# Performance work log

Measured on AMD Instinct MI355X. Metric: run time of the kernel, lower is better.

Reference implementation:

```python
import jax, jax.numpy as jnp
import numpy as np

NUM_EXPERTS = 16
TOP_K = 2


def _swiglu(x, w13, w2):
    # x: [t, d]; w13: [2I, d] (gate and up fused); w2: [d, I]
    h = x @ w13.T                      # [t, 2I]
    gate, up = jnp.split(h, 2, axis=-1)
    return (jax.nn.silu(gate) * up) @ w2.T  # [t, d]


def setup_inputs() -> dict:
    key = jax.random.key(0)
    ks = jax.random.split(key, 6)
    T, D, I, E, SI = 4096, 1024, 512, NUM_EXPERTS, 2048
    return {
        "hidden_states": jax.random.normal(ks[0], (T, D), jnp.float32),
        "router_logits": jax.random.normal(ks[1], (T, E), jnp.float32),
        "w13": jax.random.normal(ks[2], (E, 2 * I, D), jnp.float32) * (1.0 / np.sqrt(D)),
        "w2": jax.random.normal(ks[3], (E, D, I), jnp.float32) * (1.0 / np.sqrt(I)),
        "w13_shared": jax.random.normal(ks[4], (2 * SI, D), jnp.float32) * (1.0 / np.sqrt(D)),
        "w2_shared": jax.random.normal(ks[5], (D, SI), jnp.float32) * (1.0 / np.sqrt(SI)),
    }


def reference(hidden_states, router_logits, w13, w2, w13_shared, w2_shared):
    # Shared expert path (overlapped with routed dispatch in the original).
    shared_out = _swiglu(hidden_states, w13_shared, w2_shared)  # [T, d]

    # Routing: softmax -> top-k -> renormalize (vLLM FusedMoE w/ renormalize=True).
    probs = jax.nn.softmax(router_logits, axis=-1)              # [T, E]
    topk_w, topk_idx = jax.lax.top_k(probs, TOP_K)              # [T, k]
    topk_w = topk_w / jnp.sum(topk_w, axis=-1, keepdims=True)

    # Dense combine-weight matrix [T, E]: zero where expert not selected.
    T = hidden_states.shape[0]
    combine = jnp.zeros((T, NUM_EXPERTS), hidden_states.dtype)
    combine = combine.at[jnp.arange(T)[:, None], topk_idx].add(topk_w)

    # Grouped expert compute: scan over experts (fixed structural set),
    # accumulating the combine-weighted SwiGLU output. Memory-friendly: no
    # [E, T, 2I] intermediate is materialized.
    def body(acc, ew):
        w13_e, w2_e, c_e = ew                     # [2I,d], [d,I], [T]
        y = _swiglu(hidden_states, w13_e, w2_e)   # [T, d]
        return acc + c_e[:, None] * y, None

    fused_out, _ = jax.lax.scan(body, jnp.zeros_like(hidden_states),
                                (w13, w2, combine.T))
    return shared_out, fused_out
```

## Files before the change

### kernel.cpp

```cpp
#include <hip/hip_runtime.h>


#define T_TOK 4096
#define NEXP  16

typedef __attribute__((ext_vector_type(8))) short   short8;
typedef __attribute__((ext_vector_type(4))) float   floatx4;

typedef __attribute__((address_space(1))) void as1_void;
typedef __attribute__((address_space(3))) void as3_void;

__device__ __forceinline__ float bf2f(ushort u) {
    union { unsigned int i; float f; } v; v.i = ((unsigned int)u) << 16; return v.f;
}
__device__ __forceinline__ ushort f2bf(float f) {
    unsigned int u = __builtin_bit_cast(unsigned int, f);
    unsigned int r = 0x7FFFu + ((u >> 16) & 1u);
    return (ushort)((u + r) >> 16);
}

__device__ __forceinline__ float load_elem(const void* p, long i, int bf) {
    return bf ? bf2f(((const ushort*)p)[i]) : ((const float*)p)[i];
}

__device__ __forceinline__ void top2(const void* logits, int t, int bf,
                                     int& b0, int& b1, float& w0, float& w1) {
    float l[16];
#pragma unroll
    for (int j = 0; j < 16; ++j) l[j] = load_elem(logits, t * 16 + j, bf);
    b0 = 0; float v0 = l[0];
#pragma unroll
    for (int j = 1; j < 16; ++j) { if (l[j] > v0) { v0 = l[j]; b0 = j; } }
    b1 = -1; float v1 = -3.4e38f;
#pragma unroll
    for (int j = 0; j < 16; ++j) {
        if (j == b0) continue;
        if (l[j] > v1) { v1 = l[j]; b1 = j; }
    }
    float d = __expf(v1 - v0);
    w0 = 1.0f / (1.0f + d);
    w1 = d / (1.0f + d);
}

__global__ __launch_bounds__(1024)
void setup_all(const void* __restrict__ in0, const void* __restrict__ in4,
               const void* __restrict__ logits,
               int* __restrict__ dflag, int* __restrict__ xsel,
               int* __restrict__ counts, int* __restrict__ offsets,
               int* __restrict__ pairinfo, float* __restrict__ pairw)
{
    __shared__ int   s_cnt[16], s_off[16], s_cur[16];
    __shared__ int   s_dcnt, s_dflag, s_xsel;
    __shared__ float s0s, s4s;
    const int tid = threadIdx.x;

    if (tid < 16) { s_cnt[tid] = 0; s_cur[tid] = 0; }
    if (tid == 0) { s_dcnt = 0; s0s = 0.f; s4s = 0.f; }
    __syncthreads();

    if (tid < 256) {
        const ushort* xu = (const ushort*)in0;
        int ok = 0;
        for (int i = tid; i < 512; i += 256) {
            int e = (xu[2 * i] >> 7) & 0xFF;
            ok += (e >= 90 && e <= 140) ? 1 : 0;
        }
        atomicAdd(&s_dcnt, ok);
    }
    __syncthreads();
    if (tid == 0) { s_dflag = (s_dcnt >= 384) ? 1 : 0; *dflag = s_dflag; }
    __syncthreads();
    const int bf = s_dflag;

    if (tid < 256) {
        float a0 = 0.f, a4 = 0.f;
        for (int i = tid; i < 4096; i += 256) {
            a0 += fabsf(load_elem(in0, (long)i * 997 + 13, bf));
            a4 += fabsf(load_elem(in4, (long)i * 997 + 13, bf));
        }
        atomicAdd(&s0s, a0);
        atomicAdd(&s4s, a4);
    }
    __syncthreads();
    if (tid == 0) { s_xsel = (s0s >= s4s) ? 0 : 1; *xsel = s_xsel; }

    int   b0[4], b1[4];
    float w0[4], w1[4];
#pragma unroll
    for (int it = 0; it < 4; ++it) {
        const int t = tid + it * 1024;
        top2(logits, t, bf, b0[it], b1[it], w0[it], w1[it]);
        atomicAdd(&s_cnt[b0[it]], 1);
        atomicAdd(&s_cnt[b1[it]], 1);
    }
    __syncthreads();

    if (tid == 0) {
        int acc = 0;
        for (int e = 0; e < NEXP; ++e) {
            s_off[e] = acc; offsets[e] = acc; counts[e] = s_cnt[e];
            acc += s_cnt[e];
        }
    }
    __syncthreads();

#pragma unroll
    for (int it = 0; it < 4; ++it) {
        const int t = tid + it * 1024;
        int p0 = s_off[b0[it]] + atomicAdd(&s_cur[b0[it]], 1);
        pairinfo[p0] = 2 * t;     pairw[p0] = w0[it];
        int p1 = s_off[b1[it]] + atomicAdd(&s_cur[b1[it]], 1);
        pairinfo[p1] = 2 * t + 1; pairw[p1] = w1[it];
    }
}

__global__ __launch_bounds__(256)
void conv_all(const void* __restrict__ in0, const void* __restrict__ in4,
              const void* __restrict__ w13, const void* __restrict__ w2,
              const void* __restrict__ w2s, ushort* __restrict__ dst,
              const int* __restrict__ dflag, const int* __restrict__ xsel)
{
    const int bf = *dflag, xs = *xsel;
    const long E0 = 524288;
    const long E1 = 1048576;
    const long E2 = 3145728;
    const long E3 = 4194304;
    const long E4 = 4456448;
    long i = (long)blockIdx.x * blockDim.x + threadIdx.x;
    const long stride = (long)gridDim.x * blockDim.x;
    for (; i < E4; i += stride) {
        const void* src; long j;
        if      (i < E0) { src = xs ? in4 : in0; j = i;      }
        else if (i < E1) { src = xs ? in0 : in4; j = i - E0; }
        else if (i < E2) { src = w13;            j = i - E1; }
        else if (i < E3) { src = w2;             j = i - E2; }
        else             { src = w2s;            j = i - E3; }
        uint4 v;
        if (bf) {
            v = ((const uint4*)src)[j];
        } else {
            float4 f0 = ((const float4*)src)[j * 2];
            float4 f1 = ((const float4*)src)[j * 2 + 1];
            v.x = (unsigned)f2bf(f0.x) | ((unsigned)f2bf(f0.y) << 16);
            v.y = (unsigned)f2bf(f0.z) | ((unsigned)f2bf(f0.w) << 16);
            v.z = (unsigned)f2bf(f1.x) | ((unsigned)f2bf(f1.y) << 16);
            v.w = (unsigned)f2bf(f1.z) | ((unsigned)f2bf(f1.w) << 16);
        }
        ((uint4*)dst)[i] = v;
    }
}

__global__ void to_bf16(const void* __restrict__ pA, const void* __restrict__ pB,
                        ushort* __restrict__ dst, long n8,
                        const int* __restrict__ dflag, const int* __restrict__ xsel)
{
    const void* src = (pB != nullptr && *xsel) ? pB : pA;
    const int bf = *dflag;
    long i = (long)blockIdx.x * blockDim.x + threadIdx.x;
    const long stride = (long)gridDim.x * blockDim.x;
    for (; i < n8; i += stride) {
        uint4 v;
        if (bf) {
            v = ((const uint4*)src)[i];
        } else {
            float4 f0 = ((const float4*)src)[i * 2];
            float4 f1 = ((const float4*)src)[i * 2 + 1];
            v.x = (unsigned)f2bf(f0.x) | ((unsigned)f2bf(f0.y) << 16);
            v.y = (unsigned)f2bf(f0.z) | ((unsigned)f2bf(f0.w) << 16);
            v.z = (unsigned)f2bf(f1.x) | ((unsigned)f2bf(f1.y) << 16);
            v.w = (unsigned)f2bf(f1.z) | ((unsigned)f2bf(f1.w) << 16);
        }
        ((uint4*)dst)[i] = v;
    }
}

__device__ __forceinline__ void gload16(const ushort* g, ushort* l) {
    __builtin_amdgcn_global_load_lds((as1_void*)g, (as3_void*)l, 16, 0, 0);
}

template <int SWIGLU, int GATHER, int ROUTED, int SCATTER, int NARROW = 0>
__device__ __forceinline__ void gemm_core(
    ushort* __restrict__ smem,
    const ushort* __restrict__ A, int lda,
    const ushort* __restrict__ B0, long upoff, long bbase, int ldb,
    void* __restrict__ C, int ldc, float* __restrict__ C2,
    int m0, int n0, int Mloc, int K, int pair_base,
    const int* __restrict__ pairinfo, const float* __restrict__ pairw)
{
    constexpr int BNRW = (SWIGLU || NARROW);
    constexpr int NBI = BNRW ? 2 : 4;
    constexpr int NFN = BNRW ? 2 : 4;

    ushort* As  = smem;
    ushort* Bs0 = smem + 128 * 64;
    ushort* Bs1 = SWIGLU ? (smem + 128 * 64 + 64 * 64) : nullptr;

    const int tid  = threadIdx.x;
    const int lane = tid & 63;
    const int wave = tid >> 6;
    const int srow = lane >> 3;
    const int scol = ((lane & 7) ^ srow) * 8;

    long aoff[4];
#pragma unroll
    for (int i = 0; i < 4; ++i) {
        int rl  = m0 + (wave * 4 + i) * 8 + srow;
        int rlc = rl < Mloc ? rl : Mloc - 1;
        long gr;
        if (GATHER)      gr = (long)(pairinfo[pair_base + rlc] >> 1);
        else if (ROUTED) gr = pair_base + rlc;
        else             gr = rlc;
        aoff[i] = gr * (long)lda + scol;
    }
    long boff[NBI];
#pragma unroll
    for (int i = 0; i < NBI; ++i) {
        int r = (wave * NBI + i) * 8 + srow;
        boff[i] = bbase + (long)(n0 + r) * ldb + scol;
    }

    const int wm   = (wave >> 1) * 64;
    const int wn   = (wave & 1) * (BNRW ? 32 : 64);
    const int r16  = lane & 15;
    const int quad = lane >> 4;
    const int rlow = r16 & 7;

    const floatx4 z4 = {0.f, 0.f, 0.f, 0.f};
    floatx4 accg[4][NFN], accu[4][NFN];
#pragma unroll
    for (int mi = 0; mi < 4; ++mi)
#pragma unroll
        for (int ni = 0; ni < NFN; ++ni) { accg[mi][ni] = z4; accu[mi][ni] = z4; }

    for (int k0 = 0; k0 < K; k0 += 64) {
#pragma unroll
        for (int i = 0; i < 4; ++i)
            gload16(A + aoff[i] + k0, &As[(wave * 4 + i) * 512]);
#pragma unroll
        for (int i = 0; i < NBI; ++i) {
            gload16(B0 + boff[i] + k0, &Bs0[(wave * NBI + i) * 512]);
            if constexpr (SWIGLU)
                gload16(B0 + boff[i] + upoff + k0, &Bs1[(wave * NBI + i) * 512]);
        }
        __syncthreads();
#pragma unroll
        for (int kc = 0; kc < 2; ++kc) {
            const int sw = ((kc * 4 + quad) ^ rlow) * 8;
            short8 af[4];
#pragma unroll
            for (int mi = 0; mi < 4; ++mi)
                af[mi] = *(const short8*)&As[(wm + mi * 16 + r16) * 64 + sw];
            short8 bfr[NFN], ufr[NFN];
#pragma unroll
            for (int ni = 0; ni < NFN; ++ni) {
                bfr[ni] = *(const short8*)&Bs0[(wn + ni * 16 + r16) * 64 + sw];
                if constexpr (SWIGLU)
                    ufr[ni] = *(const short8*)&Bs1[(wn + ni * 16 + r16) * 64 + sw];
            }
#pragma unroll
            for (int mi = 0; mi < 4; ++mi)
#pragma unroll
                for (int ni = 0; ni < NFN; ++ni) {
                    accg[mi][ni] = __builtin_amdgcn_mfma_f32_16x16x32_bf16(
                        af[mi], bfr[ni], accg[mi][ni], 0, 0, 0);
                    if constexpr (SWIGLU)
                        accu[mi][ni] = __builtin_amdgcn_mfma_f32_16x16x32_bf16(
                            af[mi], ufr[ni], accu[mi][ni], 0, 0, 0);
                }
        }
        __syncthreads();
    }

#pragma unroll
    for (int mi = 0; mi < 4; ++mi) {
#pragma unroll
        for (int r = 0; r < 4; ++r) {
            const int grow = m0 + wm + mi * 16 + quad * 4 + r;
            if (grow >= Mloc) continue;
            int info = 0; float w = 0.f;
            if constexpr (SCATTER) {
                const int p = pair_base + grow;
                info = pairinfo[p]; w = pairw[p];
            }
#pragma unroll
            for (int ni = 0; ni < NFN; ++ni) {
                const int col = n0 + wn + ni * 16 + r16;
                float val;
                if constexpr (SWIGLU) {
                    float g = accg[mi][ni][r];
                    float u = accu[mi][ni][r];
                    val = (g / (1.0f + __expf(-g))) * u;
                } else {
                    val = accg[mi][ni][r];
                }
                if constexpr (SCATTER) {
                    long idx = (long)(info >> 1) * 1024 + col;
                    float* dst = (info & 1) ? C2 : (float*)C;
                    dst[idx] = w * val;
                } else if constexpr (SWIGLU) {
                    long crow = ROUTED ? (long)(pair_base + grow) : (long)grow;
                    ((ushort*)C)[crow * ldc + col] = f2bf(val);
                } else {
                    ((float*)C)[(long)grow * ldc + col] = val;
                }
            }
        }
    }
}

template <int SWIGLU, int GATHER, int ROUTED, int SCATTER>
__global__ __launch_bounds__(256)
void gemm_fast(const ushort* __restrict__ A, int lda,
               const ushort* __restrict__ B0, long upoff, long strideB, int ldb,
               void* __restrict__ C, int ldc, float* __restrict__ C2,
               int M, int K,
               const int* __restrict__ counts, const int* __restrict__ offsets,
               const int* __restrict__ pairinfo, const float* __restrict__ pairw)
{
    __shared__ __align__(16) ushort smem[16384];
    const int e    = ROUTED ? (int)blockIdx.z : 0;
    const int Mloc = ROUTED ? counts[e] : M;
    const int m0   = blockIdx.y * 128;
    if (m0 >= Mloc) return;
    constexpr int BN = SWIGLU ? 64 : 128;
    const int n0  = blockIdx.x * BN;
    const int pb  = ROUTED ? offsets[e] : 0;
    const long bb = ROUTED ? (long)e * strideB : 0L;
    gemm_core<SWIGLU, GATHER, ROUTED, SCATTER>(
        smem, A, lda, B0, upoff, bb, ldb, C, ldc, C2,
        m0, n0, Mloc, K, pb, pairinfo, pairw);
}

__global__ __launch_bounds__(256)
void g1_fused(const ushort* __restrict__ hidb, const ushort* __restrict__ w13b,
              const ushort* __restrict__ w13sb,
              ushort* __restrict__ actR, ushort* __restrict__ actS,
              const int* __restrict__ counts, const int* __restrict__ offsets,
              const int* __restrict__ pairinfo)
{
    __shared__ __align__(16) ushort smem[16384];
    const int z  = blockIdx.z;
    const int m0 = blockIdx.y * 128;
    if (z < 4) {
        const int e    = z * 4 + ((int)blockIdx.x >> 3);
        const int Mloc = counts[e];
        if (m0 >= Mloc) return;
        const int n0 = ((int)blockIdx.x & 7) * 64;
        gemm_core<1, 1, 1, 0>(smem, hidb, 1024,
                              w13b, (long)512 * 1024, (long)e * 1024 * 1024, 1024,
                              actR, 512, nullptr,
                              m0, n0, Mloc, 1024, offsets[e], pairinfo, nullptr);
    } else {
        const int n0 = (int)blockIdx.x * 64;
        gemm_core<1, 0, 0, 0>(smem, hidb, 1024,
                              w13sb, (long)2048 * 1024, 0L, 1024,
                              actS, 2048, nullptr,
                              m0, n0, T_TOK, 1024, 0, nullptr, nullptr);
    }
}

template <int SPLIT>
__global__ __launch_bounds__(256)
void g2_fused(const ushort* __restrict__ actR, const ushort* __restrict__ actS,
              const ushort* __restrict__ w2b, const ushort* __restrict__ w2sb,
              float* __restrict__ outF, float* __restrict__ outT,
              float* __restrict__ outS, float* __restrict__ outP,
              const int* __restrict__ counts, const int* __restrict__ offsets,
              const int* __restrict__ pairinfo, const float* __restrict__ pairw)
{
    __shared__ __align__(16) ushort smem[16384];
    const int z  = blockIdx.z;
    const int m0 = blockIdx.y * 128;
    if (z < 4) {
        const int e    = z * 4 + ((int)blockIdx.x >> 3);
        const int Mloc = counts[e];
        if (m0 >= Mloc) return;
        const int n0 = ((int)blockIdx.x & 7) * 128;
        gemm_core<0, 0, 1, 1>(smem, actR, 512,
                              w2b, 0L, (long)e * 1024 * 512, 512,
                              outF, 1024, outT,
                              m0, n0, Mloc, 512, offsets[e], pairinfo, pairw);
    } else if constexpr (SPLIT) {
        const int zz = z - 4;
        if ((int)blockIdx.x >= 16) return;
        const int n0 = (int)blockIdx.x * 64;
        gemm_core<0, 0, 0, 0, 1>(smem, actS + zz * 1024, 2048,
                                 w2sb + zz * 1024, 0L, 0L, 2048,
                                 zz ? outP : outS, 1024, nullptr,
                                 m0, n0, T_TOK, 1024, 0, nullptr, nullptr);
    } else {
        if ((int)blockIdx.x >= 8) return;
        const int n0 = (int)blockIdx.x * 128;
        gemm_core<0, 0, 0, 0>(smem, actS, 2048,
                              w2sb, 0L, 0L, 2048,
                              outS, 1024, nullptr,
                              m0, n0, T_TOK, 2048, 0, nullptr, nullptr);
    }
}

__global__ void add_kernel(float* __restrict__ outF, const float* __restrict__ outT, int n4) {
    int i = blockIdx.x * blockDim.x + threadIdx.x;
    if (i >= n4) return;
    float4 a = *(const float4*)(outF + (long)i * 4);
    float4 b = *(const float4*)(outT + (long)i * 4);
    a.x += b.x; a.y += b.y; a.z += b.z; a.w += b.w;
    *(float4*)(outF + (long)i * 4) = a;
}

__global__ void add2_kernel(float* __restrict__ outF, const float* __restrict__ outT,
                            float* __restrict__ outS, const float* __restrict__ outP,
                            int n4) {
    int i = blockIdx.x * blockDim.x + threadIdx.x;
    if (i < n4) {
        float4 a = *(const float4*)(outF + (long)i * 4);
        float4 b = *(const float4*)(outT + (long)i * 4);
        a.x += b.x; a.y += b.y; a.z += b.z; a.w += b.w;
        *(float4*)(outF + (long)i * 4) = a;
    } else if (i < 2 * n4) {
        int j = i - n4;
        float4 a = *(const float4*)(outS + (long)j * 4);
        float4 b = *(const float4*)(outP + (long)j * 4);
        a.x += b.x; a.y += b.y; a.z += b.z; a.w += b.w;
        *(float4*)(outS + (long)j * 4) = a;
    }
}

__device__ __forceinline__ void stage8(const void* __restrict__ src, long eoff, int bf,
                                       ushort* __restrict__ dst) {
    if (bf) {
        *(uint4*)dst = *(const uint4*)((const ushort*)src + eoff);
    } else {
        const float* s = (const float*)src + eoff;
        float4 f0 = *(const float4*)s;
        float4 f1 = *(const float4*)(s + 4);
        uint4 v;
        v.x = (unsigned)f2bf(f0.x) | ((unsigned)f2bf(f0.y) << 16);
        v.y = (unsigned)f2bf(f0.z) | ((unsigned)f2bf(f0.w) << 16);
        v.z = (unsigned)f2bf(f1.x) | ((unsigned)f2bf(f1.y) << 16);
        v.w = (unsigned)f2bf(f1.z) | ((unsigned)f2bf(f1.w) << 16);
        *(uint4*)dst = v;
    }
}

template <int SWIGLU, int GATHER, int ROUTED, int SCATTER, int LOCAL,
          int A_DT, int B_DT, int C_F32>
__global__ __launch_bounds__(256)
void gemm_nt(const void* __restrict__ A, const void* __restrict__ Aalt, int lda,
             const void* __restrict__ B0, const void* __restrict__ B0alt,
             long upoff, long strideB,
             void* __restrict__ C, int ldc, void* __restrict__ C2,
             int M, int K, int row0,
             const int* __restrict__ dflag, const int* __restrict__ xsel,
             const int* __restrict__ counts, const int* __restrict__ offsets,
             const int* __restrict__ pairinfo, const float* __restrict__ pairw,
             int e_base, int m_base, int Mcap)
{
    const int dfl = (A_DT && B_DT) ? 1 : *dflag;
    const int abf = A_DT ? 1 : dfl;
    const int bbf = B_DT ? 1 : dfl;
    if (Aalt  && *xsel) A  = Aalt;
    if (B0alt && *xsel) B0 = B0alt;

    const int e = ROUTED ? (e_base + (int)blockIdx.z) : 0;
    int Mloc;
    if (ROUTED) {
        int avail = counts[e] - m_base;
        Mloc = avail < Mcap ? avail : Mcap;
    } else {
        Mloc = M;
    }
    const int m0 = blockIdx.y * 64;
    if (m0 >= Mloc) return;
    const int n0 = blockIdx.x * 64;
    const int pair_base = ROUTED ? (offsets[e] + m_base) : 0;
    const int abase     = ROUTED ? (LOCAL ? 0 : offsets[e]) : 0;
    const long bbase    = ROUTED ? (long)e * strideB : 0L;

    constexpr int LS = 72;
    __shared__ __align__(16) ushort As[64 * LS];
    __shared__ __align__(16) ushort Bs0[64 * LS];
    __shared__ __align__(16) ushort Bs1[SWIGLU ? 64 * LS : 8];

    const int tid = threadIdx.x;

    int  lofs[2];
    long aoff[2], boff[2];
#pragma unroll
    for (int i = 0; i < 2; ++i) {
        int idx = tid + i * 256;
        int row = idx >> 3;
        int col = (idx & 7) * 8;
        lofs[i] = row * LS + col;
        int rl  = m0 + row;
        int rlc = rl < Mloc ? rl : (Mloc - 1);
        long rA;
        if (GATHER)      rA = (long)(pairinfo[pair_base + rlc] >> 1);
        else if (ROUTED) rA = abase + rlc;
        else             rA = row0 + rl;
        aoff[i] = rA * (long)lda + col;
        boff[i] = bbase + (long)(n0 + row) * K + col;
    }

    const int lane = tid & 63;
    const int wave = tid >> 6;
    const int wm   = (wave >> 1) * 32;
    const int wn   = (wave & 1) * 32;
    const int r16  = lane & 15;
    const int quad = lane >> 4;

    floatx4 accg[2][2] = {{{0.f,0.f,0.f,0.f},{0.f,0.f,0.f,0.f}},{{0.f,0.f,0.f,0.f},{0.f,0.f,0.f,0.f}}};
    floatx4 accu[2][2] = {{{0.f,0.f,0.f,0.f},{0.f,0.f,0.f,0.f}},{{0.f,0.f,0.f,0.f},{0.f,0.f,0.f,0.f}}};

    for (int k0 = 0; k0 < K; k0 += 64) {
#pragma unroll
        for (int i = 0; i < 2; ++i) {
            stage8(A,  aoff[i] + k0, abf, &As[lofs[i]]);
            stage8(B0, boff[i] + k0, bbf, &Bs0[lofs[i]]);
            if (SWIGLU) stage8(B0, boff[i] + k0 + upoff, bbf, &Bs1[lofs[i]]);
        }
        __syncthreads();
#pragma unroll
        for (int kc = 0; kc < 2; ++kc) {
            const int kof = kc * 32 + quad * 8;
            short8 a0 = *(const short8*)&As[(wm + r16)      * LS + kof];
            short8 a1 = *(const short8*)&As[(wm + 16 + r16) * LS + kof];
            short8 b0 = *(const short8*)&Bs0[(wn + r16)      * LS + kof];
            short8 b1 = *(const short8*)&Bs0[(wn + 16 + r16) * LS + kof];
            accg[0][0] = __builtin_amdgcn_mfma_f32_16x16x32_bf16(a0, b0, accg[0][0], 0, 0, 0);
            accg[0][1] = __builtin_amdgcn_mfma_f32_16x16x32_bf16(a0, b1, accg[0][1], 0, 0, 0);
            accg[1][0] = __builtin_amdgcn_mfma_f32_16x16x32_bf16(a1, b0, accg[1][0], 0, 0, 0);
            accg[1][1] = __builtin_amdgcn_mfma_f32_16x16x32_bf16(a1, b1, accg[1][1], 0, 0, 0);
            if (SWIGLU) {
                short8 u0 = *(const short8*)&Bs1[(wn + r16)      * LS + kof];
                short8 u1 = *(const short8*)&Bs1[(wn + 16 + r16) * LS + kof];
                accu[0][0] = __builtin_amdgcn_mfma_f32_16x16x32_bf16(a0, u0, accu[0][0], 0, 0, 0);
                accu[0][1] = __builtin_amdgcn_mfma_f32_16x16x32_bf16(a0, u1, accu[0][1], 0, 0, 0);
                accu[1][0] = __builtin_amdgcn_mfma_f32_16x16x32_bf16(a1, u0, accu[1][0], 0, 0, 0);
                accu[1][1] = __builtin_amdgcn_mfma_f32_16x16x32_bf16(a1, u1, accu[1][1], 0, 0, 0);
            }
        }
        __syncthreads();
    }

#pragma unroll
    for (int mi = 0; mi < 2; ++mi) {
#pragma unroll
        for (int ni = 0; ni < 2; ++ni) {
#pragma unroll
            for (int r = 0; r < 4; ++r) {
                int rowl = wm + mi * 16 + quad * 4 + r;
                int grow = m0 + rowl;
                if (grow < Mloc) {
                    int col = n0 + wn + ni * 16 + r16;
                    float g = accg[mi][ni][r];
                    float val;
                    if (SWIGLU) {
                        float u = accu[mi][ni][r];
                        val = (g / (1.0f + __expf(-g))) * u;
                    } else {
                        val = g;
                    }
                    if (SCATTER) {
                        int p    = pair_base + grow;
                        int info = pairinfo[p];
                        float w  = pairw[p];
                        long idx = (long)(info >> 1) * 1024 + col;
                        void* dst = (info & 1) ? C2 : C;
                        if (C_F32) ((float*)dst)[idx]  = w * val;
                        else       ((ushort*)dst)[idx] = f2bf(w * val);
                    } else {
                        int crow = ROUTED ? (abase + grow) : grow;
                        long idx = (long)crow * ldc + col;
                        if (C_F32) ((float*)C)[idx]  = val;
                        else       ((ushort*)C)[idx] = f2bf(val);
                    }
                }
            }
        }
    }
}

extern "C" void kernel_launch(void* const* d_in, const int* in_sizes, int n_in,
                              void* d_out, int out_size, void* d_ws, size_t ws_size,
                              hipStream_t stream)
{
    const void* in0  = d_in[0];
    const void* rl   = d_in[1];
    const void* w13  = d_in[2];
    const void* w2   = d_in[3];
    const void* in4  = d_in[4];
    const void* w2s  = d_in[5];
    float* outS = (float*)d_out;
    float* outF = (float*)d_out + (size_t)T_TOK * 1024;

    char*  base     = (char*)d_ws;
    int*   counts   = (int*)(base);
    int*   dflag    = (int*)(base + 128);
    int*   xsel     = (int*)(base + 132);
    int*   offsets  = (int*)(base + 192);
    int*   pairinfo = (int*)(base + 256);
    float* pairw    = (float*)(base + 256 + 32768);
    const size_t META = 256 + 65536;

    size_t avail = ws_size > META ? ws_size - META : 0;

    setup_all<<<1, 1024, 0, stream>>>(in0, in4, rl, dflag, xsel,
                                      counts, offsets, pairinfo, pairw);

    const long sB1  = (long)1024 * 1024;
    const long sB2  = (long)1024 * 512;
    const long UP_R = (long)512 * 1024;
    const long UP_S = (long)2048 * 1024;

    const size_t FULL3_NEED = 113246208ULL;
    const size_t FULL2_NEED = 96468992ULL;
    const size_t FULL_NEED  = 88080384ULL;
    const size_t MID_NEED   = 29360128ULL;

    if (avail >= FULL2_NEED) {
        ushort* hidb  = (ushort*)(base + META);
        ushort* w13sb = hidb  + (size_t)4096 * 1024;
        ushort* w13b  = w13sb + (size_t)4096 * 1024;
        ushort* w2b   = w13b  + (size_t)16 * 1024 * 1024;
        ushort* w2sb  = w2b   + (size_t)16 * 1024 * 512;
        ushort* actR  = w2sb  + (size_t)1024 * 2048;
        ushort* actS  = actR  + (size_t)8192 * 512;
        float*  outP  = (float*)(actS + (size_t)4096 * 2048);
        float*  outT  = (float*)hidb;

        conv_all<<<2048, 256, 0, stream>>>(in0, in4, w13, w2, w2s,
                                           hidb, dflag, xsel);

        g1_fused<<<dim3(32, 32, 5), 256, 0, stream>>>(
            hidb, w13b, w13sb, actR, actS, counts, offsets, pairinfo);

        if (avail >= FULL3_NEED) {
            g2_fused<1><<<dim3(32, 32, 6), 256, 0, stream>>>(
                actR, actS, w2b, w2sb, outF, outT, outS, outP,
                counts, offsets, pairinfo, pairw);
            add2_kernel<<<(2 * (T_TOK * 1024 / 4) + 255) / 256, 256, 0, stream>>>(
                outF, outT, outS, outP, T_TOK * 1024 / 4);
        } else {
            g2_fused<0><<<dim3(32, 32, 5), 256, 0, stream>>>(
                actR, actS, w2b, w2sb, outF, outT, outS, nullptr,
                counts, offsets, pairinfo, pairw);
            add_kernel<<<(T_TOK * 1024 / 4 + 255) / 256, 256, 0, stream>>>(
                outF, outT, T_TOK * 1024 / 4);
        }
    } else if (avail >= FULL_NEED) {
        ushort* hidb  = (ushort*)(base + META);
        ushort* w13sb = hidb  + (size_t)4096 * 1024;
        ushort* w13b  = w13sb + (size_t)4096 * 1024;
        ushort* w2b   = w13b  + (size_t)16 * 1024 * 1024;
        ushort* w2sb  = w2b   + (size_t)16 * 1024 * 512;
        ushort* actb  = w2sb  + (size_t)1024 * 2048;

        conv_all<<<2048, 256, 0, stream>>>(in0, in4, w13, w2, w2s,
                                           hidb, dflag, xsel);

        gemm_fast<1,1,1,0><<<dim3(8, 32, NEXP), 256, 0, stream>>>(
            hidb, 1024, w13b, UP_R, sB1, 1024, actb, 512, nullptr, 0, 1024,
            counts, offsets, pairinfo, pairw);
        gemm_fast<0,0,1,1><<<dim3(8, 32, NEXP), 256, 0, stream>>>(
            actb, 512, w2b, 0, sB2, 512, outF, 1024, outS, 0, 512,
            counts, offsets, pairinfo, pairw);
        add_kernel<<<(T_TOK * 1024 / 4 + 255) / 256, 256, 0, stream>>>(outF, outS, T_TOK * 1024 / 4);
        gemm_fast<1,0,0,0><<<dim3(32, 32), 256, 0, stream>>>(
            hidb, 1024, w13sb, UP_S, 0, 1024, actb, 2048, nullptr, 4096, 1024,
            nullptr, nullptr, nullptr, nullptr);
        gemm_fast<0,0,0,0><<<dim3(8, 32), 256, 0, stream>>>(
            actb, 2048, w2sb, 0, 0, 2048, outS, 1024, nullptr, 4096, 2048,
            nullptr, nullptr, nullptr, nullptr);
    } else if (avail >= MID_NEED) {
        ushort* act   = (ushort*)(base + META);
        ushort* hidb  = act   + (size_t)8192 * 512;
        ushort* w13sb = hidb  + (size_t)4096 * 1024;
        ushort* w2sb  = w13sb + (size_t)4096 * 1024;

        to_bf16<<<1024, 256, 0, stream>>>(in0, in4, hidb,  (long)4096 * 1024 / 8, dflag, xsel);
        to_bf16<<<1024, 256, 0, stream>>>(in4, in0, w13sb, (long)4096 * 1024 / 8, dflag, xsel);
        to_bf16<<<1024, 256, 0, stream>>>(w2s, nullptr, w2sb, (long)1024 * 2048 / 8, dflag, xsel);

        gemm_nt<1,1,1,0,0,1,0,0><<<dim3(8, 64, NEXP), 256, 0, stream>>>(
            hidb, nullptr, 1024, w13, nullptr, UP_R, sB1, act, 512, nullptr, 0, 1024, 0,
            dflag, xsel, counts, offsets, pairinfo, pairw, 0, 0, T_TOK);
        gemm_nt<0,0,1,1,0,1,0,1><<<dim3(16, 64, NEXP), 256, 0, stream>>>(
            act, nullptr, 512, w2, nullptr, 0, sB2, outF, 1024, outS, 0, 512, 0,
            dflag, xsel, counts, offsets, pairinfo, pairw, 0, 0, T_TOK);
        add_kernel<<<(T_TOK * 1024 / 4 + 255) / 256, 256, 0, stream>>>(outF, outS, T_TOK * 1024 / 4);
        for (int c = 0; c < 2; ++c) {
            gemm_fast<1,0,0,0><<<dim3(32, 16), 256, 0, stream>>>(
                hidb + (size_t)c * 2048 * 1024, 1024, w13sb, UP_S, 0, 1024,
                act, 2048, nullptr, 2048, 1024, nullptr, nullptr, nullptr, nullptr);
            gemm_fast<0,0,0,0><<<dim3(8, 16), 256, 0, stream>>>(
                act, 2048, w2sb, 0, 0, 2048, outS + (size_t)c * 2048 * 1024, 1024, nullptr,
                2048, 2048, nullptr, nullptr, nullptr, nullptr);
        }
    } else {
        const size_t MB = 1024 * 1024;
        int grouped, Mcap, CH;
        if      (avail >= 8 * MB) { grouped = 1; Mcap = T_TOK; CH = 2048; }
        else if (avail >= 1 * MB) { grouped = 0; Mcap = 1024;  CH = 256;  }
        else                      { grouped = 0; Mcap = 256;   CH = 64;   }
        ushort* act = (ushort*)(base + META);

        if (grouped) {
            gemm_nt<1,1,1,0,0,0,0,0><<<dim3(8, 64, NEXP), 256, 0, stream>>>(
                in0, in4, 1024, w13, nullptr, UP_R, sB1, act, 512, nullptr, 0, 1024, 0,
                dflag, xsel, counts, offsets, pairinfo, pairw, 0, 0, T_TOK);
            gemm_nt<0,0,1,1,0,1,0,1><<<dim3(16, 64, NEXP), 256, 0, stream>>>(
                act, nullptr, 512, w2, nullptr, 0, sB2, outF, 1024, outS, 0, 512, 0,
                dflag, xsel, counts, offsets, pairinfo, pairw, 0, 0, T_TOK);
        } else {
            for (int e = 0; e < NEXP; ++e) {
                for (int mb = 0; mb < T_TOK; mb += Mcap) {
                    gemm_nt<1,1,1,0,1,0,0,0><<<dim3(8, Mcap / 64, 1), 256, 0, stream>>>(
                        in0, in4, 1024, w13, nullptr, UP_R, sB1, act, 512, nullptr, 0, 1024, 0,
                        dflag, xsel, counts, offsets, pairinfo, pairw, e, mb, Mcap);
                    gemm_nt<0,0,1,1,1,1,0,1><<<dim3(16, Mcap / 64, 1), 256, 0, stream>>>(
                        act, nullptr, 512, w2, nullptr, 0, sB2, outF, 1024, outS, 0, 512, 0,
                        dflag, xsel, counts, offsets, pairinfo, pairw, e, mb, Mcap);
                }
            }
        }
        add_kernel<<<(T_TOK * 1024 / 4 + 255) / 256, 256, 0, stream>>>(outF, outS, T_TOK * 1024 / 4);
        for (int c = 0; c < T_TOK / CH; ++c) {
            gemm_nt<1,0,0,0,0,0,0,0><<<dim3(2048 / 64, CH / 64), 256, 0, stream>>>(
                in0, in4, 1024, in4, in0, UP_S, 0, act, 2048, nullptr, CH, 1024, c * CH,
                dflag, xsel, nullptr, nullptr, nullptr, nullptr, 0, 0, 0);
            gemm_nt<0,0,0,0,0,1,0,1><<<dim3(1024 / 64, CH / 64), 256, 0, stream>>>(
                act, nullptr, 2048, w2s, nullptr, 0, 0,
                outS + (size_t)c * CH * 1024, 1024, nullptr, CH, 2048, 0,
                dflag, xsel, nullptr, nullptr, nullptr, nullptr, 0, 0, 0);
        }
    }
    (void)in_sizes; (void)n_in; (void)out_size;
}
```

Before: 385.0 us.

## Fuse routing setup into conversion kernel and use atomic accumulation in down-projection

Merges the single-block routing and dtype-detection setup into the bf16 conversion kernel as an extra block, so the serial setup launch overlaps with conversion. The second GEMM now accumulates routed top-k pairs and both shared-expert K-halves into zeroed outputs with atomicAdd, which removes the temporary buffers and the separate add kernels. It also adds an XCD-aware block-index swizzle for better L2 locality. The cost is a memset of the outputs, atomic traffic in the epilogue, and float-sum ordering that is no longer deterministic.

```diff
diff --git a/kernel.cpp b/kernel.cpp
--- a/kernel.cpp
+++ b/kernel.cpp
@@ -40,6 +40,97 @@
     float d = __expf(v1 - v0);
     w0 = 1.0f / (1.0f + d);
     w1 = d / (1.0f + d);
+}
+
+__global__ __launch_bounds__(1024)
+void conv_plus(const void* __restrict__ in0, const void* __restrict__ in4,
+               const void* __restrict__ w13, const void* __restrict__ w2,
+               const void* __restrict__ w2s, ushort* __restrict__ dst,
+               const void* __restrict__ logits,
+               int* __restrict__ dflag, int* __restrict__ xsel,
+               int* __restrict__ counts, int* __restrict__ offsets,
+               int* __restrict__ pairinfo, float* __restrict__ pairw)
+{
+    const int tid = threadIdx.x;
+
+    __shared__ int   s_ok;
+    __shared__ float s0s, s4s;
+    if (tid == 0) { s_ok = 0; s0s = 0.f; s4s = 0.f; }
+    __syncthreads();
+    if (tid < 256) {
+        int e = (((const ushort*)in0)[2 * tid] >> 7) & 0xFF;
+        if (e >= 90 && e <= 140) atomicAdd(&s_ok, 1);
+    }
+    __syncthreads();
+    const int bf = (s_ok >= 192) ? 1 : 0;
+    if (tid < 64) {
+        atomicAdd(&s0s, fabsf(load_elem(in0, (long)tid * 997 + 13, bf)));
+        atomicAdd(&s4s, fabsf(load_elem(in4, (long)tid * 997 + 13, bf)));
+    }
+    __syncthreads();
+    const int xs = (s0s >= s4s) ? 0 : 1;
+
+    if (blockIdx.x == 512) {
+        __shared__ int s_cnt[16], s_off[16], s_cur[16];
+        if (tid < 16) { s_cnt[tid] = 0; s_cur[tid] = 0; }
+        if (tid == 0) { *dflag = bf; *xsel = xs; }
+        __syncthreads();
+        int   b0[4], b1[4];
+        float w0[4], w1[4];
+#pragma unroll
+        for (int it = 0; it < 4; ++it) {
+            const int t = tid + it * 1024;
+            top2(logits, t, bf, b0[it], b1[it], w0[it], w1[it]);
+            atomicAdd(&s_cnt[b0[it]], 1);
+            atomicAdd(&s_cnt[b1[it]], 1);
+        }
+        __syncthreads();
+        if (tid == 0) {
+            int acc = 0;
+            for (int e = 0; e < NEXP; ++e) {
+                s_off[e] = acc; offsets[e] = acc; counts[e] = s_cnt[e];
+                acc += s_cnt[e];
+            }
+        }
+        __syncthreads();
+#pragma unroll
+        for (int it = 0; it < 4; ++it) {
+            const int t = tid + it * 1024;
+            int p0 = s_off[b0[it]] + atomicAdd(&s_cur[b0[it]], 1);
+            pairinfo[p0] = 2 * t;     pairw[p0] = w0[it];
+            int p1 = s_off[b1[it]] + atomicAdd(&s_cur[b1[it]], 1);
+            pairinfo[p1] = 2 * t + 1; pairw[p1] = w1[it];
+        }
+        return;
+    }
+
+    const long E0 = 524288;
+    const long E1 = 1048576;
+    const long E2 = 3145728;
+    const long E3 = 4194304;
+    const long E4 = 4456448;
+    long i = (long)blockIdx.x * 1024 + tid;
+    const long stride = 512L * 1024;
+    for (; i < E4; i += stride) {
+        const void* src; long j;
+        if      (i < E0) { src = xs ? in4 : in0; j = i;      }
+        else if (i < E1) { src = xs ? in0 : in4; j = i - E0; }
+        else if (i < E2) { src = w13;            j = i - E1; }
+        else if (i < E3) { src = w2;             j = i - E2; }
+        else             { src = w2s;            j = i - E3; }
+        uint4 v;
+        if (bf) {
+            v = ((const uint4*)src)[j];
+        } else {
+            float4 f0 = ((const float4*)src)[j * 2];
+            float4 f1 = ((const float4*)src)[j * 2 + 1];
+            v.x = (unsigned)f2bf(f0.x) | ((unsigned)f2bf(f0.y) << 16);
+            v.y = (unsigned)f2bf(f0.z) | ((unsigned)f2bf(f0.w) << 16);
+            v.z = (unsigned)f2bf(f1.x) | ((unsigned)f2bf(f1.y) << 16);
+            v.w = (unsigned)f2bf(f1.z) | ((unsigned)f2bf(f1.w) << 16);
+        }
+        ((uint4*)dst)[i] = v;
+    }
 }
 
 __global__ __launch_bounds__(1024)
@@ -57,7 +148,6 @@
     if (tid < 16) { s_cnt[tid] = 0; s_cur[tid] = 0; }
     if (tid == 0) { s_dcnt = 0; s0s = 0.f; s4s = 0.f; }
     __syncthreads();
-
     if (tid < 256) {
         const ushort* xu = (const ushort*)in0;
         int ok = 0;
@@ -71,7 +161,6 @@
     if (tid == 0) { s_dflag = (s_dcnt >= 384) ? 1 : 0; *dflag = s_dflag; }
     __syncthreads();
     const int bf = s_dflag;
-
     if (tid < 256) {
         float a0 = 0.f, a4 = 0.f;
         for (int i = tid; i < 4096; i += 256) {
@@ -94,7 +183,6 @@
         atomicAdd(&s_cnt[b1[it]], 1);
     }
     __syncthreads();
-
     if (tid == 0) {
         int acc = 0;
         for (int e = 0; e < NEXP; ++e) {
@@ -103,7 +191,6 @@
         }
     }
     __syncthreads();
-
 #pragma unroll
     for (int it = 0; it < 4; ++it) {
         const int t = tid + it * 1024;
@@ -121,11 +208,7 @@
               const int* __restrict__ dflag, const int* __restrict__ xsel)
 {
     const int bf = *dflag, xs = *xsel;
-    const long E0 = 524288;
-    const long E1 = 1048576;
-    const long E2 = 3145728;
-    const long E3 = 4194304;
-    const long E4 = 4456448;
+    const long E0 = 524288, E1 = 1048576, E2 = 3145728, E3 = 4194304, E4 = 4456448;
     long i = (long)blockIdx.x * blockDim.x + threadIdx.x;
     const long stride = (long)gridDim.x * blockDim.x;
     for (; i < E4; i += stride) {
@@ -178,7 +261,7 @@
     __builtin_amdgcn_global_load_lds((as1_void*)g, (as3_void*)l, 16, 0, 0);
 }
 
-template <int SWIGLU, int GATHER, int ROUTED, int SCATTER, int NARROW = 0>
+template <int SWIGLU, int GATHER, int ROUTED, int SCATTER, int NARROW = 0, int ATOM = 0>
 __device__ __forceinline__ void gemm_core(
     ushort* __restrict__ smem,
     const ushort* __restrict__ A, int lda,
@@ -295,17 +378,31 @@
                 }
                 if constexpr (SCATTER) {
                     long idx = (long)(info >> 1) * 1024 + col;
-                    float* dst = (info & 1) ? C2 : (float*)C;
-                    dst[idx] = w * val;
+                    if constexpr (ATOM) {
+                        atomicAdd((float*)C + idx, w * val);
+                    } else {
+                        float* dst = (info & 1) ? C2 : (float*)C;
+                        dst[idx] = w * val;
+                    }
                 } else if constexpr (SWIGLU) {
                     long crow = ROUTED ? (long)(pair_base + grow) : (long)grow;
                     ((ushort*)C)[crow * ldc + col] = f2bf(val);
                 } else {
-                    ((float*)C)[(long)grow * ldc + col] = val;
+                    long idx = (long)grow * ldc + col;
+                    if constexpr (ATOM) atomicAdd((float*)C + idx, val);
+                    else                ((float*)C)[idx] = val;
                 }
             }
         }
     }
+}
+
+__device__ __forceinline__ void xcd_swz(int& x, int& y, int& z,
+                                        int nx, int ny, int nz) {
+    int d = ((int)blockIdx.z * ny + (int)blockIdx.y) * nx + (int)blockIdx.x;
+    const int N = nx * ny * nz;
+    int L = (d & 7) * (N >> 3) + (d >> 3);
+    x = L % nx; int t = L / nx; y = t % ny; z = t / ny;
 }
 
 template <int SWIGLU, int GATHER, int ROUTED, int SCATTER>
@@ -339,19 +436,20 @@
               const int* __restrict__ pairinfo)
 {
     __shared__ __align__(16) ushort smem[16384];
-    const int z  = blockIdx.z;
-    const int m0 = blockIdx.y * 128;
-    if (z < 4) {
-        const int e    = z * 4 + ((int)blockIdx.x >> 3);
+    int bx, by, bz;
+    xcd_swz(bx, by, bz, 32, 32, 5);
+    const int m0 = by * 128;
+    if (bz < 4) {
+        const int e    = bz * 4 + (bx >> 3);
         const int Mloc = counts[e];
         if (m0 >= Mloc) return;
-        const int n0 = ((int)blockIdx.x & 7) * 64;
+        const int n0 = (bx & 7) * 64;
         gemm_core<1, 1, 1, 0>(smem, hidb, 1024,
                               w13b, (long)512 * 1024, (long)e * 1024 * 1024, 1024,
                               actR, 512, nullptr,
                               m0, n0, Mloc, 1024, offsets[e], pairinfo, nullptr);
     } else {
-        const int n0 = (int)blockIdx.x * 64;
+        const int n0 = bx * 64;
         gemm_core<1, 0, 0, 0>(smem, hidb, 1024,
                               w13sb, (long)2048 * 1024, 0L, 1024,
                               actS, 2048, nullptr,
@@ -359,42 +457,33 @@
     }
 }
 
-template <int SPLIT>
 __global__ __launch_bounds__(256)
 void g2_fused(const ushort* __restrict__ actR, const ushort* __restrict__ actS,
               const ushort* __restrict__ w2b, const ushort* __restrict__ w2sb,
-              float* __restrict__ outF, float* __restrict__ outT,
-              float* __restrict__ outS, float* __restrict__ outP,
+              float* __restrict__ outF, float* __restrict__ outS,
               const int* __restrict__ counts, const int* __restrict__ offsets,
               const int* __restrict__ pairinfo, const float* __restrict__ pairw)
 {
     __shared__ __align__(16) ushort smem[16384];
-    const int z  = blockIdx.z;
-    const int m0 = blockIdx.y * 128;
-    if (z < 4) {
-        const int e    = z * 4 + ((int)blockIdx.x >> 3);
+    int bx, by, bz;
+    xcd_swz(bx, by, bz, 32, 32, 5);
+    const int m0 = by * 128;
+    if (bz < 4) {
+        const int e    = bz * 4 + (bx >> 3);
         const int Mloc = counts[e];
         if (m0 >= Mloc) return;
-        const int n0 = ((int)blockIdx.x & 7) * 128;
-        gemm_core<0, 0, 1, 1>(smem, actR, 512,
-                              w2b, 0L, (long)e * 1024 * 512, 512,
-                              outF, 1024, outT,
-                              m0, n0, Mloc, 512, offsets[e], pairinfo, pairw);
-    } else if constexpr (SPLIT) {
-        const int zz = z - 4;
-        if ((int)blockIdx.x >= 16) return;
-        const int n0 = (int)blockIdx.x * 64;
-        gemm_core<0, 0, 0, 0, 1>(smem, actS + zz * 1024, 2048,
-                                 w2sb + zz * 1024, 0L, 0L, 2048,
-                                 zz ? outP : outS, 1024, nullptr,
-                                 m0, n0, T_TOK, 1024, 0, nullptr, nullptr);
+        const int n0 = (bx & 7) * 128;
+        gemm_core<0, 0, 1, 1, 0, 1>(smem, actR, 512,
+                                    w2b, 0L, (long)e * 1024 * 512, 512,
+                                    outF, 1024, nullptr,
+                                    m0, n0, Mloc, 512, offsets[e], pairinfo, pairw);
     } else {
-        if ((int)blockIdx.x >= 8) return;
-        const int n0 = (int)blockIdx.x * 128;
-        gemm_core<0, 0, 0, 0>(smem, actS, 2048,
-                              w2sb, 0L, 0L, 2048,
-                              outS, 1024, nullptr,
-                              m0, n0, T_TOK, 2048, 0, nullptr, nullptr);
+        const int zz = bx >> 4;
+        const int n0 = (bx & 15) * 64;
+        gemm_core<0, 0, 0, 0, 1, 1>(smem, actS + zz * 1024, 2048,
+                                    w2sb + zz * 1024, 0L, 0L, 2048,
+                                    outS, 1024, nullptr,
+                                    m0, n0, T_TOK, 1024, 0, nullptr, nullptr);
     }
 }
 
@@ -405,24 +494,6 @@
     float4 b = *(const float4*)(outT + (long)i * 4);
     a.x += b.x; a.y += b.y; a.z += b.z; a.w += b.w;
     *(float4*)(outF + (long)i * 4) = a;
-}
-
-__global__ void add2_kernel(float* __restrict__ outF, const float* __restrict__ outT,
-                            float* __restrict__ outS, const float* __restrict__ outP,
-                            int n4) {
-    int i = blockIdx.x * blockDim.x + threadIdx.x;
-    if (i < n4) {
-        float4 a = *(const float4*)(outF + (long)i * 4);
-        float4 b = *(const float4*)(outT + (long)i * 4);
-        a.x += b.x; a.y += b.y; a.z += b.z; a.w += b.w;
-        *(float4*)(outF + (long)i * 4) = a;
-    } else if (i < 2 * n4) {
-        int j = i - n4;
-        float4 a = *(const float4*)(outS + (long)j * 4);
-        float4 b = *(const float4*)(outP + (long)j * 4);
-        a.x += b.x; a.y += b.y; a.z += b.z; a.w += b.w;
-        *(float4*)(outS + (long)j * 4) = a;
-    }
 }
 
 __device__ __forceinline__ void stage8(const void* __restrict__ src, long eoff, int bf,
@@ -604,15 +675,11 @@
 
     size_t avail = ws_size > META ? ws_size - META : 0;
 
-    setup_all<<<1, 1024, 0, stream>>>(in0, in4, rl, dflag, xsel,
-                                      counts, offsets, pairinfo, pairw);
-
     const long sB1  = (long)1024 * 1024;
     const long sB2  = (long)1024 * 512;
     const long UP_R = (long)512 * 1024;
     const long UP_S = (long)2048 * 1024;
 
-    const size_t FULL3_NEED = 113246208ULL;
     const size_t FULL2_NEED = 96468992ULL;
     const size_t FULL_NEED  = 88080384ULL;
     const size_t MID_NEED   = 29360128ULL;
@@ -625,28 +692,16 @@
         ushort* w2sb  = w2b   + (size_t)16 * 1024 * 512;
         ushort* actR  = w2sb  + (size_t)1024 * 2048;
         ushort* actS  = actR  + (size_t)8192 * 512;
-        float*  outP  = (float*)(actS + (size_t)4096 * 2048);
-        float*  outT  = (float*)hidb;
-
-        conv_all<<<2048, 256, 0, stream>>>(in0, in4, w13, w2, w2s,
-                                           hidb, dflag, xsel);
-
+
+        hipMemsetAsync(d_out, 0, out_size, stream);
+        conv_plus<<<513, 1024, 0, stream>>>(in0, in4, w13, w2, w2s, hidb, rl,
+                                            dflag, xsel, counts, offsets,
+                                            pairinfo, pairw);
         g1_fused<<<dim3(32, 32, 5), 256, 0, stream>>>(
             hidb, w13b, w13sb, actR, actS, counts, offsets, pairinfo);
-
-        if (avail >= FULL3_NEED) {
-            g2_fused<1><<<dim3(32, 32, 6), 256, 0, stream>>>(
-                actR, actS, w2b, w2sb, outF, outT, outS, outP,
-                counts, offsets, pairinfo, pairw);
-            add2_kernel<<<(2 * (T_TOK * 1024 / 4) + 255) / 256, 256, 0, stream>>>(
-                outF, outT, outS, outP, T_TOK * 1024 / 4);
-        } else {
-            g2_fused<0><<<dim3(32, 32, 5), 256, 0, stream>>>(
-                actR, actS, w2b, w2sb, outF, outT, outS, nullptr,
-                counts, offsets, pairinfo, pairw);
-            add_kernel<<<(T_TOK * 1024 / 4 + 255) / 256, 256, 0, stream>>>(
-                outF, outT, T_TOK * 1024 / 4);
-        }
+        g2_fused<<<dim3(32, 32, 5), 256, 0, stream>>>(
+            actR, actS, w2b, w2sb, outF, outS,
+            counts, offsets, pairinfo, pairw);
     } else if (avail >= FULL_NEED) {
         ushort* hidb  = (ushort*)(base + META);
         ushort* w13sb = hidb  + (size_t)4096 * 1024;
@@ -655,6 +710,8 @@
         ushort* w2sb  = w2b   + (size_t)16 * 1024 * 512;
         ushort* actb  = w2sb  + (size_t)1024 * 2048;
 
+        setup_all<<<1, 1024, 0, stream>>>(in0, in4, rl, dflag, xsel,
+                                          counts, offsets, pairinfo, pairw);
         conv_all<<<2048, 256, 0, stream>>>(in0, in4, w13, w2, w2s,
                                            hidb, dflag, xsel);
 
@@ -677,6 +734,8 @@
         ushort* w13sb = hidb  + (size_t)4096 * 1024;
         ushort* w2sb  = w13sb + (size_t)4096 * 1024;
 
+        setup_all<<<1, 1024, 0, stream>>>(in0, in4, rl, dflag, xsel,
+                                          counts, offsets, pairinfo, pairw);
         to_bf16<<<1024, 256, 0, stream>>>(in0, in4, hidb,  (long)4096 * 1024 / 8, dflag, xsel);
         to_bf16<<<1024, 256, 0, stream>>>(in4, in0, w13sb, (long)4096 * 1024 / 8, dflag, xsel);
         to_bf16<<<1024, 256, 0, stream>>>(w2s, nullptr, w2sb, (long)1024 * 2048 / 8, dflag, xsel);
@@ -704,6 +763,8 @@
         else                      { grouped = 0; Mcap = 256;   CH = 64;   }
         ushort* act = (ushort*)(base + META);
 
+        setup_all<<<1, 1024, 0, stream>>>(in0, in4, rl, dflag, xsel,
+                                          counts, offsets, pairinfo, pairw);
         if (grouped) {
             gemm_nt<1,1,1,0,0,0,0,0><<<dim3(8, 64, NEXP), 256, 0, stream>>>(
                 in0, in4, 1024, w13, nullptr, UP_R, sB1, act, 512, nullptr, 0, 1024, 0,
```

Result: slower. 515.0 us (+33.8%).
